# Optimization experiments

Measured on AMD Instinct MI355X. Metric: run time of the kernel, lower is better.

Reference implementation:

```python
import jax, jax.numpy as jnp
import numpy as np

D_MODEL = 1024
NUM_HEADS = 16
D_K = D_MODEL // NUM_HEADS
THETA = 10000.0
B, S = 2, 2048


def setup_inputs() -> dict:
    key = jax.random.key(0)
    k_x, k_q, k_k, k_v, k_o = jax.random.split(key, 5)
    std = np.sqrt(2.0 / (D_MODEL + D_MODEL))
    x = jax.random.normal(k_x, (B, S, D_MODEL), dtype=jnp.float32)
    # positions: per-row arange 0..S-1 (must stay < max_seq_len)
    token_positions = jnp.broadcast_to(jnp.arange(S, dtype=jnp.int32), (B, S))
    mk = lambda k: (jax.random.normal(k, (D_MODEL, D_MODEL), dtype=jnp.float32) * std)
    return {
        'x': x,
        'token_positions': token_positions,
        'Wq': mk(k_q), 'Wk': mk(k_k), 'Wv': mk(k_v), 'Wo': mk(k_o),
    }


def _rope(x, pos):
    # x: [B, H, S, D_K], pos: [B, S] int
    inv_freq = 1.0 / (THETA ** (jnp.arange(0, D_K, 2, dtype=jnp.float32) / D_K))  # [D_K/2]
    angles = pos.astype(jnp.float32)[..., None] * inv_freq  # [B, S, D_K/2]
    cos = jnp.cos(angles)[:, None, :, :]  # [B, 1, S, D_K/2]
    sin = jnp.sin(angles)[:, None, :, :]
    x_even = x[..., 0::2]
    x_odd = x[..., 1::2]
    out_even = x_even * cos - x_odd * sin
    out_odd = x_even * sin + x_odd * cos
    # interleave back: [..., D_K/2, 2] -> [..., D_K]
    return jnp.stack([out_even, out_odd], axis=-1).reshape(x.shape)


def reference(x, token_positions, Wq, Wk, Wv, Wo):
    b, s, d = x.shape
    h, dk = NUM_HEADS, D_K
    # projections: weight is [d_out, d_in], y = x W^T
    q = jnp.einsum('bsd,ed->bse', x, Wq).reshape(b, s, h, dk).transpose(0, 2, 1, 3)
    k = jnp.einsum('bsd,ed->bse', x, Wk).reshape(b, s, h, dk).transpose(0, 2, 1, 3)
    v = jnp.einsum('bsd,ed->bse', x, Wv).reshape(b, s, h, dk).transpose(0, 2, 1, 3)
    q = _rope(q, token_positions)
    k = _rope(k, token_positions)
    scores = jnp.einsum('bhqd,bhkd->bhqk', q, k) / jnp.sqrt(jnp.float32(dk))
    causal = jnp.tril(jnp.ones((s, s), dtype=bool))
    scores = jnp.where(causal, scores, -jnp.inf)
    weights = jax.nn.softmax(scores, axis=-1)
    attn = jnp.einsum('bhqk,bhkd->bhqd', weights, v)  # [B,H,S,D_K]
    concat = attn.transpose(0, 2, 1, 3).reshape(b, s, d)
    return jnp.einsum('bsd,ed->bse', concat, Wo)
```

## Files before the change

### kernel.cpp

```cpp
#include <hip/hip_runtime.h>
#include <hip/hip_bf16.h>

#define BB 2
#define SS 2048
#define DD 1024
#define HH 16
#define DKK 64
#define MM (BB * SS)
#define PER ((size_t)MM * DD)

typedef __bf16 v8bf __attribute__((ext_vector_type(8)));
typedef float  v4f  __attribute__((ext_vector_type(4)));

__device__ __forceinline__ float bf2f(unsigned int u16) {
    union { unsigned int i; float f; } x;
    x.i = u16 << 16;
    return x.f;
}
__device__ __forceinline__ unsigned int pack2(float a, float b) {
    union { __hip_bfloat16 h; unsigned short u; } x, y;
    x.h = __float2bfloat16(a); y.h = __float2bfloat16(b);
    return (unsigned int)x.u | ((unsigned int)y.u << 16);
}
__device__ __forceinline__ unsigned short f2bfu(float v) {
    union { __hip_bfloat16 h; unsigned short u; } x;
    x.h = __float2bfloat16(v);
    return x.u;
}
template<bool BF>
__device__ __forceinline__ void ld4(const void* p, size_t i, float* f) {
    if (BF) {
        const uint2 u = *(const uint2*)((const unsigned short*)p + i);
        f[0] = bf2f(u.x & 0xffffu); f[1] = bf2f(u.x >> 16);
        f[2] = bf2f(u.y & 0xffffu); f[3] = bf2f(u.y >> 16);
    } else {
        const float4 v = *(const float4*)((const float*)p + i);
        f[0] = v.x; f[1] = v.y; f[2] = v.z; f[3] = v.w;
    }
}
template<bool BF>
__device__ __forceinline__ void st1(void* p, size_t i, float v) {
    if (BF) ((__hip_bfloat16*)p)[i] = __float2bfloat16(v);
    else    ((float*)p)[i] = v;
}
template<bool BF>
__device__ __forceinline__ uint4 ld8bf(const void* p, size_t i) {
    if (BF) return *(const uint4*)((const unsigned short*)p + i);
    float f[8];
    ld4<false>(p, i, f);
    ld4<false>(p, i + 4, f + 4);
    uint4 u;
    u.x = pack2(f[0], f[1]); u.y = pack2(f[2], f[3]);
    u.z = pack2(f[4], f[5]); u.w = pack2(f[6], f[7]);
    return u;
}

typedef const __attribute__((address_space(1))) void* gas_p;
typedef __attribute__((address_space(3))) void* las_p;
__device__ __forceinline__ void gld16(const void* g, void* l) {
    __builtin_amdgcn_global_load_lds(
        (gas_p)(unsigned long long)g,
        (las_p)(unsigned int)(unsigned long long)l,
        16, 0, 0);
}

__device__ __forceinline__ bool sniff_bf(const void* x) {
    const unsigned int w = ((const unsigned int*)x)[threadIdx.x & 63];
    const int e = (w >> 7) & 0xFF;
    return __popcll(__ballot(e >= 100 && e <= 140)) >= 32;
}

__global__ __launch_bounds__(256) void precast(
    const void* __restrict__ X,  const void* __restrict__ Wq,
    const void* __restrict__ Wk, const void* __restrict__ Wv,
    const void* __restrict__ Wo, unsigned short* __restrict__ out)
{
    const int bid = blockIdx.x;
    const int tid = threadIdx.x;
    const void* src;
    size_t off;
    unsigned short* dst;
    if (bid < 2048) {
        src = X;
        off = (size_t)bid * 2048;
        dst = out + off;
    } else {
        const int w  = (bid - 2048) >> 9;
        const size_t lo = (size_t)((bid - 2048) & 511) * 2048;
        src = (w == 0) ? Wq : (w == 1) ? Wk : (w == 2) ? Wv : Wo;
        off = lo;
        dst = out + PER + (size_t)w * (DD * DD) + lo;
    }
    const bool bf = sniff_bf(src);
    const size_t i = off + (size_t)tid * 8;
    if (bf) {
        *(uint4*)(dst + tid * 8) = *(const uint4*)((const unsigned short*)src + i);
    } else {
        float f[8];
        ld4<false>(src, i, f);
        ld4<false>(src, i + 4, f + 4);
        uint4 u;
        u.x = pack2(f[0], f[1]); u.y = pack2(f[2], f[3]);
        u.z = pack2(f[4], f[5]); u.w = pack2(f[6], f[7]);
        *(uint4*)(dst + tid * 8) = u;
    }
}

template<bool BF>
__device__ __forceinline__ void qkv_body128(
    const void* __restrict__ X,
    const void* __restrict__ Wq, const void* __restrict__ Wk, const void* __restrict__ Wv,
    const int* __restrict__ pos,
    __hip_bfloat16* __restrict__ Qb, __hip_bfloat16* __restrict__ Kb,
    __hip_bfloat16* __restrict__ Vb,
    unsigned short* Sh)
{
    const int tid  = threadIdx.x;
    const int lane = tid & 63;
    const int wv   = tid >> 6;
    const int wr   = wv >> 1;
    const int wc   = wv & 1;
    const int ln   = lane & 15;
    const int qd   = lane >> 4;
    const int r8   = lane >> 3;
    const int pc   = lane & 7;
    const int lchunk = pc ^ r8;

    const int m0  = blockIdx.x * 128;
    const int n0g = blockIdx.y * 128;
    const int z   = n0g >> 10;
    const int nw  = n0g & (DD - 1);
    const void* W = (z == 0) ? Wq : (z == 1) ? Wk : Wv;

    unsigned short* As = Sh;
    unsigned short* Bs = Sh + 128 * 64;

    v4f acc[4][4];
#pragma unroll
    for (int i = 0; i < 4; ++i)
#pragma unroll
        for (int j = 0; j < 4; ++j) acc[i][j] = (v4f){0.f, 0.f, 0.f, 0.f};

    for (int k0 = 0; k0 < DD; k0 += 64) {
        __syncthreads();
#pragma unroll
        for (int g = 0; g < 4; ++g) {
            const int base = (wv * 4 + g) * 8;
            const int row  = base + r8;
            const size_t ga = (size_t)(m0 + row) * DD + k0 + lchunk * 8;
            if (BF) gld16((const unsigned short*)X + ga, As + (size_t)base * 64);
            else    *(uint4*)(As + (size_t)row * 64 + pc * 8) = ld8bf<false>(X, ga);
            const size_t gb = (size_t)(nw + row) * DD + k0 + lchunk * 8;
            if (BF) gld16((const unsigned short*)W + gb, Bs + (size_t)base * 64);
            else    *(uint4*)(Bs + (size_t)row * 64 + pc * 8) = ld8bf<false>(W, gb);
        }
        __syncthreads();
#pragma unroll
        for (int h = 0; h < 2; ++h) {
            v8bf a[4], b[4];
#pragma unroll
            for (int mt = 0; mt < 4; ++mt)
                a[mt] = *(const v8bf*)&As[(size_t)(wr * 64 + mt * 16 + ln) * 64 +
                                          (((h * 4 + qd) ^ (ln & 7))) * 8];
#pragma unroll
            for (int nt = 0; nt < 4; ++nt)
                b[nt] = *(const v8bf*)&Bs[(size_t)(wc * 64 + nt * 16 + ln) * 64 +
                                          (((h * 4 + qd) ^ (ln & 7))) * 8];
#pragma unroll
            for (int mt = 0; mt < 4; ++mt)
#pragma unroll
                for (int nt = 0; nt < 4; ++nt)
                    acc[mt][nt] = __builtin_amdgcn_mfma_f32_16x16x32_bf16(
                        a[mt], b[nt], acc[mt][nt], 0, 0, 0);
        }
    }

    const int bb = m0 >> 11;
    if (z < 2) {
        __hip_bfloat16* Out = z ? Kb : Qb;
        const int head = (nw >> 6) + wc;
        float invf[4];
#pragma unroll
        for (int nt = 0; nt < 4; ++nt) {
            const int dk = nt * 16 + ln;
            invf[nt] = __expf((float)(dk >> 1) * -0.2878231366f);
        }
#pragma unroll
        for (int mt = 0; mt < 4; ++mt) {
#pragma unroll
            for (int r = 0; r < 4; ++r) {
                const int m = m0 + wr * 64 + mt * 16 + qd * 4 + r;
                const int s = m & (SS - 1);
                const float p = (float)pos[m];
#pragma unroll
                for (int nt = 0; nt < 4; ++nt) {
                    const int dk = nt * 16 + ln;
                    const float val = acc[mt][nt][r];
                    const float ang = p * invf[nt];
                    float sn, cs;
                    __sincosf(ang, &sn, &cs);
                    const float prt = __shfl_xor(val, 1);
                    float res = ((dk & 1) == 0) ? (val * cs - prt * sn)
                                                : (prt * sn + val * cs);
                    if (z == 0) res *= 0.125f;
                    Out[((size_t)(bb * HH + head) * SS + s) * DKK + dk] =
                        __float2bfloat16(res);
                }
            }
        }
    } else {
        const int s0 = m0 & (SS - 1);
#pragma unroll
        for (int h2 = 0; h2 < 2; ++h2) {
            __syncthreads();
            if (wc == h2) {
#pragma unroll
                for (int nt = 0; nt < 4; ++nt)
#pragma unroll
                    for (int mt = 0; mt < 4; ++mt)
#pragma unroll
                        for (int r = 0; r < 4; ++r)
                            Sh[(size_t)(nt * 16 + ln) * 136 +
                               wr * 64 + mt * 16 + qd * 4 + r] =
                                f2bfu(acc[mt][nt][r]);
            }
            __syncthreads();
            const int head = (nw >> 6) + h2;
            const int row  = tid >> 2;
            const int c    = (tid & 3) * 32;
            unsigned short* dst = (unsigned short*)Vb +
                ((size_t)(bb * HH + head) * DKK + row) * SS + s0 + c;
            const unsigned short* Ts = Sh + (size_t)row * 136 + c;
#pragma unroll
            for (int j = 0; j < 4; ++j)
                *(uint4*)(dst + j * 8) = *(const uint4*)(Ts + j * 8);
        }
    }
}

__global__ __launch_bounds__(256) void qkv_gemm(
    const void* __restrict__ X,
    const void* __restrict__ Wq, const void* __restrict__ Wk, const void* __restrict__ Wv,
    const int* __restrict__ pos,
    __hip_bfloat16* __restrict__ Qb, __hip_bfloat16* __restrict__ Kb,
    __hip_bfloat16* __restrict__ Vb)
{
    __shared__ unsigned short Sh[128 * 64 * 2];
    if (sniff_bf(X)) qkv_body128<true>(X, Wq, Wk, Wv, pos, Qb, Kb, Vb, Sh);
    else             qkv_body128<false>(X, Wq, Wk, Wv, pos, Qb, Kb, Vb, Sh);
}

__global__ __launch_bounds__(256) void qkv_gemm_pc(
    const unsigned short* __restrict__ Xb,
    const unsigned short* __restrict__ Wqb, const unsigned short* __restrict__ Wkb,
    const unsigned short* __restrict__ Wvb,
    const int* __restrict__ pos,
    __hip_bfloat16* __restrict__ Qb, __hip_bfloat16* __restrict__ Kb,
    __hip_bfloat16* __restrict__ Vb)
{
    __shared__ unsigned short Sh[128 * 64 * 2];
    qkv_body128<true>(Xb, Wqb, Wkb, Wvb, pos, Qb, Kb, Vb, Sh);
}

__global__ __launch_bounds__(256) void attn_kernel(
    const __hip_bfloat16* __restrict__ Qb,
    const __hip_bfloat16* __restrict__ Kb,
    const __hip_bfloat16* __restrict__ Vtb,
    unsigned short* __restrict__ Ob, int olay)
{
    __shared__ unsigned short Ks[2][64 * 64];
    __shared__ unsigned short Vs[2][64 * 64];
    __shared__ unsigned short Ps[4][16 * 72];

    const int tid  = threadIdx.x;
    const int bh   = blockIdx.x & 31;
    const int qt   = 31 - (blockIdx.x >> 5);
    const int q0   = qt * 64;
    const int lane = tid & 63;
    const int wv   = tid >> 6;
    const int ln   = lane & 15;
    const int qd   = lane >> 4;
    const int r8   = lane >> 3;
    const int pc   = lane & 7;
    const int lchunk = pc ^ r8;

    const unsigned short* Qu = (const unsigned short*)Qb + (size_t)bh * SS * DKK;
    const unsigned short* Ku = (const unsigned short*)Kb + (size_t)bh * SS * DKK;
    const unsigned short* Vu = (const unsigned short*)Vtb + (size_t)bh * DKK * SS;

    const int qrow = q0 + wv * 16 + ln;
    const v8bf qf0 = *(const v8bf*)(Qu + (size_t)qrow * DKK + qd * 8);
    const v8bf qf1 = *(const v8bf*)(Qu + (size_t)qrow * DKK + 32 + qd * 8);

    auto stage = [&](int t, int b) {
        const int k0 = t * 64;
#pragma unroll
        for (int g = 0; g < 2; ++g) {
            const int row  = wv * 16 + g * 8 + r8;
            const int base = wv * 16 + g * 8;
            gld16(Ku + (size_t)(k0 + row) * DKK + lchunk * 8,
                  Ks[b] + (size_t)base * 64);
            gld16(Vu + (size_t)row * SS + k0 + lchunk * 8,
                  Vs[b] + (size_t)base * 64);
        }
    };

    v4f oacc[4];
#pragma unroll
    for (int n = 0; n < 4; ++n) oacc[n] = (v4f){0.f, 0.f, 0.f, 0.f};
    float lsum = 0.f;

    const int ntiles = qt + 1;
    const int qi = q0 + wv * 16 + ln;

    stage(0, 0);
    __syncthreads();

    for (int t = 0; t < ntiles; ++t) {
        const int cur = t & 1;
        if (t + 1 < ntiles) stage(t + 1, cur ^ 1);

        const unsigned short* Kc = Ks[cur];
        const unsigned short* Vc = Vs[cur];

        v4f s[4];
        __builtin_amdgcn_s_setprio(1);
#pragma unroll
        for (int g = 0; g < 4; ++g) {
            s[g] = (v4f){0.f, 0.f, 0.f, 0.f};
            const int krow = g * 16 + ln;
            const v8bf kf0 = *(const v8bf*)&Kc[(size_t)krow * 64 + ((qd ^ (ln & 7))) * 8];
            const v8bf kf1 = *(const v8bf*)&Kc[(size_t)krow * 64 + (((4 + qd) ^ (ln & 7))) * 8];
            s[g] = __builtin_amdgcn_mfma_f32_16x16x32_bf16(kf0, qf0, s[g], 0, 0, 0);
            s[g] = __builtin_amdgcn_mfma_f32_16x16x32_bf16(kf1, qf1, s[g], 0, 0, 0);
        }
        __builtin_amdgcn_s_setprio(0);

        const int k0 = t * 64;
        if (t == qt) {
#pragma unroll
            for (int g = 0; g < 4; ++g)
#pragma unroll
                for (int r = 0; r < 4; ++r) {
                    const int key = k0 + g * 16 + qd * 4 + r;
                    const float sv = (key <= qi) ? s[g][r] : -1e30f;
                    const float p = __expf(sv - 20.f);
                    s[g][r] = p;
                    lsum += p;
                }
        } else {
#pragma unroll
            for (int g = 0; g < 4; ++g)
#pragma unroll
                for (int r = 0; r < 4; ++r) {
                    const float p = __expf(s[g][r] - 20.f);
                    s[g][r] = p;
                    lsum += p;
                }
        }

        unsigned short* Pw = Ps[wv];
#pragma unroll
        for (int g = 0; g < 4; ++g) {
            uint2 w;
            w.x = pack2(s[g][0], s[g][1]);
            w.y = pack2(s[g][2], s[g][3]);
            *(uint2*)&Pw[(size_t)ln * 72 + g * 16 + qd * 4] = w;
        }

        const v8bf pf0 = *(const v8bf*)&Pw[(size_t)ln * 72 + qd * 8];
        const v8bf pf1 = *(const v8bf*)&Pw[(size_t)ln * 72 + 32 + qd * 8];
        __builtin_amdgcn_s_setprio(1);
#pragma unroll
        for (int n = 0; n < 4; ++n) {
            const int vrow = n * 16 + ln;
            const v8bf vf0 = *(const v8bf*)&Vc[(size_t)vrow * 64 + ((qd ^ (ln & 7))) * 8];
            const v8bf vf1 = *(const v8bf*)&Vc[(size_t)vrow * 64 + (((4 + qd) ^ (ln & 7))) * 8];
            oacc[n] = __builtin_amdgcn_mfma_f32_16x16x32_bf16(pf0, vf0, oacc[n], 0, 0, 0);
            oacc[n] = __builtin_amdgcn_mfma_f32_16x16x32_bf16(pf1, vf1, oacc[n], 0, 0, 0);
        }
        __builtin_amdgcn_s_setprio(0);

        __syncthreads();
    }

    lsum += __shfl_xor(lsum, 16);
    lsum += __shfl_xor(lsum, 32);

#pragma unroll
    for (int r = 0; r < 4; ++r) {
        const float inv = 1.f / __shfl(lsum, qd * 4 + r);
        const int row = q0 + wv * 16 + qd * 4 + r;
        unsigned short* op;
        if (olay) {
            op = Ob + ((size_t)((bh >> 4) * SS + row)) * DD + (bh & 15) * DKK;
        } else {
            op = Ob + ((size_t)bh * SS + row) * DKK;
        }
#pragma unroll
        for (int n = 0; n < 4; ++n)
            op[n * 16 + ln] = f2bfu(oacc[n][r] * inv);
    }
}

template<bool BFB, bool BFO, bool ACONT>
__device__ __forceinline__ void out_body128(
    const __hip_bfloat16* __restrict__ Ab, const void* __restrict__ Wo,
    void* __restrict__ Cb, float* __restrict__ Cf, int raw,
    unsigned short* Sh)
{
    const int tid  = threadIdx.x;
    const int lane = tid & 63;
    const int wv   = tid >> 6;
    const int wr   = wv >> 1;
    const int wc   = wv & 1;
    const int ln   = lane & 15;
    const int qd   = lane >> 4;
    const int r8   = lane >> 3;
    const int pc   = lane & 7;
    const int lchunk = pc ^ r8;

    const int m0 = blockIdx.x * 128, n0 = blockIdx.y * 128;
    const unsigned short* Au = (const unsigned short*)Ab;

    unsigned short* Abuf[2] = { Sh,               Sh + 2 * 8192 };
    unsigned short* Bbuf[2] = { Sh + 8192,        Sh + 3 * 8192 };

    auto stage = [&](int k0, unsigned short* Ad, unsigned short* Bd) {
#pragma unroll
        for (int g = 0; g < 4; ++g) {
            const int base = (wv * 4 + g) * 8;
            const int row  = base + r8;
            const int m = m0 + row;
            size_t ga;
            if (ACONT) ga = (size_t)m * DD + k0 + lchunk * 8;
            else       ga = ((size_t)((m >> 11) * HH + (k0 >> 6)) * SS + (m & (SS - 1))) * DKK
                            + lchunk * 8;
            gld16(Au + ga, Ad + (size_t)base * 64);
            const size_t gb = (size_t)(n0 + row) * DD + k0 + lchunk * 8;
            if (BFB) gld16((const unsigned short*)Wo + gb, Bd + (size_t)base * 64);
            else     *(uint4*)(Bd + (size_t)row * 64 + pc * 8) = ld8bf<false>(Wo, gb);
        }
    };

    v4f acc[4][4];
#pragma unroll
    for (int i = 0; i < 4; ++i)
#pragma unroll
        for (int j = 0; j < 4; ++j) acc[i][j] = (v4f){0.f, 0.f, 0.f, 0.f};

    stage(0, Abuf[0], Bbuf[0]);
    __syncthreads();

    for (int kk = 0; kk < 16; ++kk) {
        const int cur = kk & 1;
        if (kk + 1 < 16) stage((kk + 1) * 64, Abuf[cur ^ 1], Bbuf[cur ^ 1]);

        const unsigned short* As = Abuf[cur];
        const unsigned short* Bs = Bbuf[cur];
#pragma unroll
        for (int h = 0; h < 2; ++h) {
            v8bf a[4], b[4];
#pragma unroll
            for (int mt = 0; mt < 4; ++mt)
                a[mt] = *(const v8bf*)&As[(size_t)(wr * 64 + mt * 16 + ln) * 64 +
                                          (((h * 4 + qd) ^ (ln & 7))) * 8];
#pragma unroll
            for (int nt = 0; nt < 4; ++nt)
                b[nt] = *(const v8bf*)&Bs[(size_t)(wc * 64 + nt * 16 + ln) * 64 +
                                          (((h * 4 + qd) ^ (ln & 7))) * 8];
#pragma unroll
            for (int mt = 0; mt < 4; ++mt)
#pragma unroll
                for (int nt = 0; nt < 4; ++nt)
                    acc[mt][nt] = __builtin_amdgcn_mfma_f32_16x16x32_bf16(
                        a[mt], b[nt], acc[mt][nt], 0, 0, 0);
        }
        __syncthreads();
    }

#pragma unroll
    for (int mt = 0; mt < 4; ++mt) {
#pragma unroll
        for (int r = 0; r < 4; ++r) {
            const int m = m0 + wr * 64 + mt * 16 + qd * 4 + r;
#pragma unroll
            for (int nt = 0; nt < 4; ++nt) {
                const int e = n0 + wc * 64 + nt * 16 + ln;
                const size_t idx = (size_t)m * DD + e;
                const float v = acc[mt][nt][r];
                if (raw) Cf[idx] = v;
                else     st1<BFO>(Cb, idx, v);
            }
        }
    }
}

__global__ __launch_bounds__(256) void out_gemm(
    const __hip_bfloat16* __restrict__ Ab, const void* __restrict__ Wo,
    void* __restrict__ Cb, float* __restrict__ Cf, int raw,
    const void* __restrict__ xs)
{
    __shared__ unsigned short Sh[4 * 8192];
    if (sniff_bf(xs)) out_body128<true,  true,  false>(Ab, Wo, Cb, Cf, raw, Sh);
    else              out_body128<false, false, false>(Ab, Wo, Cb, Cf, raw, Sh);
}

__global__ __launch_bounds__(256) void out_gemm_pc(
    const __hip_bfloat16* __restrict__ Ab, const unsigned short* __restrict__ Wob,
    void* __restrict__ Cb, const void* __restrict__ xs)
{
    __shared__ unsigned short Sh[4 * 8192];
    if (sniff_bf(xs)) out_body128<true, true,  true>(Ab, Wob, Cb, nullptr, 0, Sh);
    else              out_body128<true, false, true>(Ab, Wob, Cb, nullptr, 0, Sh);
}

__global__ __launch_bounds__(256) void copy_cast(
    const float* __restrict__ src, void* __restrict__ dst, const void* __restrict__ xs)
{
    const bool bf = sniff_bf(xs);
    const size_t i = (size_t)blockIdx.x * 256 + threadIdx.x;
    const float v = src[i];
    if (bf) ((__hip_bfloat16*)dst)[i] = __float2bfloat16(v);
    else    ((float*)dst)[i] = v;
}

extern "C" void kernel_launch(void* const* d_in, const int* in_sizes, int n_in,
                              void* d_out, int out_size, void* d_ws, size_t ws_size,
                              hipStream_t stream) {
    (void)in_sizes; (void)n_in; (void)out_size;

    const void* x   = d_in[0];
    const int*  pos = (const int*)d_in[1];
    const void* Wq  = d_in[2];
    const void* Wk  = d_in[3];
    const void* Wv  = d_in[4];
    const void* Wo  = d_in[5];

    char* ws = (char*)d_ws;
    const size_t bpb   = PER * 2;
    const size_t wcast = (size_t)DD * DD * 2;
    const size_t need_full = 3 * bpb + bpb + 4 * wcast + 64;

    if (ws_size >= need_full) {
        __hip_bfloat16* Qb = (__hip_bfloat16*)ws;
        __hip_bfloat16* Kb = Qb + PER;
        __hip_bfloat16* Vb = Kb + PER;
        unsigned short* cast = (unsigned short*)(ws + 3 * bpb);
        unsigned short* Xb  = cast;
        unsigned short* Wqb = cast + PER;
        unsigned short* Wkb = Wqb + (size_t)DD * DD;
        unsigned short* Wvb = Wkb + (size_t)DD * DD;
        unsigned short* Wob = Wvb + (size_t)DD * DD;
        unsigned short* Obuf = Xb;

        precast<<<dim3(4096), 256, 0, stream>>>(x, Wq, Wk, Wv, Wo, cast);

        dim3 g1(MM / 128, (3 * DD) / 128);
        qkv_gemm_pc<<<g1, 256, 0, stream>>>(Xb, Wqb, Wkb, Wvb, pos, Qb, Kb, Vb);

        dim3 g2(32 * 32);
        attn_kernel<<<g2, 256, 0, stream>>>(Qb, Kb, Vb, Obuf, 1);

        dim3 g3(MM / 128, DD / 128);
        out_gemm_pc<<<g3, 256, 0, stream>>>((const __hip_bfloat16*)Obuf, Wob, d_out, x);
    } else if (ws_size >= 3 * bpb + 64) {
        __hip_bfloat16* Qb = (__hip_bfloat16*)ws;
        __hip_bfloat16* Kb = Qb + PER;
        __hip_bfloat16* Vb = Kb + PER;

        dim3 g1(MM / 128, (3 * DD) / 128);
        qkv_gemm<<<g1, 256, 0, stream>>>(x, Wq, Wk, Wv, pos, Qb, Kb, Vb);

        dim3 g2(32 * 32);
        attn_kernel<<<g2, 256, 0, stream>>>(Qb, Kb, Vb, (unsigned short*)Qb, 0);

        dim3 g3(MM / 128, DD / 128);
        out_gemm<<<g3, 256, 0, stream>>>(Qb, Wo, d_out, nullptr, 0, x);
    } else {
        __hip_bfloat16* Qb = (__hip_bfloat16*)d_out;
        __hip_bfloat16* Kb = (__hip_bfloat16*)ws;
        __hip_bfloat16* Vb = Kb + PER;
        float* Cf = (float*)ws;

        dim3 g1(MM / 128, (3 * DD) / 128);
        qkv_gemm<<<g1, 256, 0, stream>>>(x, Wq, Wk, Wv, pos, Qb, Kb, Vb);

        dim3 g2(32 * 32);
        attn_kernel<<<g2, 256, 0, stream>>>(Qb, Kb, Vb, (unsigned short*)Qb, 0);

        dim3 g3(MM / 128, DD / 128);
        out_gemm<<<g3, 256, 0, stream>>>(Qb, Wo, nullptr, Cf, 1, x);

        copy_cast<<<PER / 256, 256, 0, stream>>>(Cf, d_out, x);
    }
}
```

Baseline: 178.2 us.

## Double-buffer QKV GEMM K-loop and use precomputed RoPE sin/cos table

Restructures the QKV projection GEMM main loop to use 32-wide K tiles with double-buffered LDS, prefetching the next tile while MFMAs run on the current one, with one barrier per iteration instead of two. It also adds extra blocks to the precast kernel that fill a position-by-frequency cos/sin table, which the GEMM epilogue reads in place of computing exp and sincos per element. This is meant to hide global-to-LDS load latency and to cut transcendental work in the epilogue. In exchange the K loop runs twice as many iterations on smaller tiles, and the epilogue now does scattered table loads.

```diff
diff --git a/kernel.cpp b/kernel.cpp
--- a/kernel.cpp
+++ b/kernel.cpp
@@ -73,10 +73,24 @@
 __global__ __launch_bounds__(256) void precast(
     const void* __restrict__ X,  const void* __restrict__ Wq,
     const void* __restrict__ Wk, const void* __restrict__ Wv,
-    const void* __restrict__ Wo, unsigned short* __restrict__ out)
+    const void* __restrict__ Wo, unsigned short* __restrict__ out,
+    float* __restrict__ tab)
 {
     const int bid = blockIdx.x;
     const int tid = threadIdx.x;
+
+    if (bid >= 4096) {
+        const int idx = (bid - 4096) * 256 + tid;
+        const int s = idx >> 5;
+        const int f = idx & 31;
+        const float invf = __expf((float)f * -0.2878231366f);
+        const float ang = (float)s * invf;
+        float sn, cs;
+        __sincosf(ang, &sn, &cs);
+        ((float2*)tab)[idx] = make_float2(cs, sn);
+        return;
+    }
+
     const void* src;
     size_t off;
     unsigned short* dst;
@@ -106,11 +120,11 @@
     }
 }
 
-template<bool BF>
+template<bool BF, bool TAB>
 __device__ __forceinline__ void qkv_body128(
     const void* __restrict__ X,
     const void* __restrict__ Wq, const void* __restrict__ Wk, const void* __restrict__ Wv,
-    const int* __restrict__ pos,
+    const int* __restrict__ pos, const float* __restrict__ tab,
     __hip_bfloat16* __restrict__ Qb, __hip_bfloat16* __restrict__ Kb,
     __hip_bfloat16* __restrict__ Vb,
     unsigned short* Sh)
@@ -122,9 +136,8 @@
     const int wc   = wv & 1;
     const int ln   = lane & 15;
     const int qd   = lane >> 4;
-    const int r8   = lane >> 3;
-    const int pc   = lane & 7;
-    const int lchunk = pc ^ r8;
+    const int srow = lane >> 2;
+    const int sc4  = lane & 3;
 
     const int m0  = blockIdx.x * 128;
     const int n0g = blockIdx.y * 128;
@@ -132,8 +145,25 @@
     const int nw  = n0g & (DD - 1);
     const void* W = (z == 0) ? Wq : (z == 1) ? Wk : Wv;
 
-    unsigned short* As = Sh;
-    unsigned short* Bs = Sh + 128 * 64;
+    unsigned short* A0 = Sh;
+    unsigned short* A1 = Sh + 4096;
+    unsigned short* B0 = Sh + 8192;
+    unsigned short* B1 = Sh + 12288;
+
+    auto stage = [&](int k0, unsigned short* Ad, unsigned short* Bd) {
+#pragma unroll
+        for (int g = 0; g < 2; ++g) {
+            const int base = (wv * 2 + g) * 16;
+            const int row  = base + srow;
+            const int sc   = sc4 ^ ((row >> 1) & 3);
+            const size_t ga = (size_t)(m0 + row) * DD + k0 + sc * 8;
+            if (BF) gld16((const unsigned short*)X + ga, Ad + (size_t)base * 32);
+            else    *(uint4*)(Ad + (size_t)row * 32 + sc4 * 8) = ld8bf<false>(X, ga);
+            const size_t gb = (size_t)(nw + row) * DD + k0 + sc * 8;
+            if (BF) gld16((const unsigned short*)W + gb, Bd + (size_t)base * 32);
+            else    *(uint4*)(Bd + (size_t)row * 32 + sc4 * 8) = ld8bf<false>(W, gb);
+        }
+    };
 
     v4f acc[4][4];
 #pragma unroll
@@ -141,38 +171,35 @@
 #pragma unroll
         for (int j = 0; j < 4; ++j) acc[i][j] = (v4f){0.f, 0.f, 0.f, 0.f};
 
-    for (int k0 = 0; k0 < DD; k0 += 64) {
+    unsigned short *Ac = A0, *An = A1, *Bc = B0, *Bn = B1;
+    stage(0, Ac, Bc);
+    __syncthreads();
+
+    const int rsw = (ln >> 1) & 3;
+
+    for (int t = 0; t < 32; ++t) {
+        if (t + 1 < 32) stage((t + 1) * 32, An, Bn);
+
+        v8bf a[4], b[4];
+#pragma unroll
+        for (int mt = 0; mt < 4; ++mt)
+            a[mt] = *(const v8bf*)&Ac[(size_t)(wr * 64 + mt * 16 + ln) * 32 +
+                                      ((qd ^ rsw)) * 8];
+#pragma unroll
+        for (int nt = 0; nt < 4; ++nt)
+            b[nt] = *(const v8bf*)&Bc[(size_t)(wc * 64 + nt * 16 + ln) * 32 +
+                                      ((qd ^ rsw)) * 8];
+#pragma unroll
+        for (int mt = 0; mt < 4; ++mt)
+#pragma unroll
+            for (int nt = 0; nt < 4; ++nt)
+                acc[mt][nt] = __builtin_amdgcn_mfma_f32_16x16x32_bf16(
+                    a[mt], b[nt], acc[mt][nt], 0, 0, 0);
+
         __syncthreads();
-#pragma unroll
-        for (int g = 0; g < 4; ++g) {
-            const int base = (wv * 4 + g) * 8;
-            const int row  = base + r8;
-            const size_t ga = (size_t)(m0 + row) * DD + k0 + lchunk * 8;
-            if (BF) gld16((const unsigned short*)X + ga, As + (size_t)base * 64);
-            else    *(uint4*)(As + (size_t)row * 64 + pc * 8) = ld8bf<false>(X, ga);
-            const size_t gb = (size_t)(nw + row) * DD + k0 + lchunk * 8;
-            if (BF) gld16((const unsigned short*)W + gb, Bs + (size_t)base * 64);
-            else    *(uint4*)(Bs + (size_t)row * 64 + pc * 8) = ld8bf<false>(W, gb);
-        }
-        __syncthreads();
-#pragma unroll
-        for (int h = 0; h < 2; ++h) {
-            v8bf a[4], b[4];
-#pragma unroll
-            for (int mt = 0; mt < 4; ++mt)
-                a[mt] = *(const v8bf*)&As[(size_t)(wr * 64 + mt * 16 + ln) * 64 +
-                                          (((h * 4 + qd) ^ (ln & 7))) * 8];
-#pragma unroll
-            for (int nt = 0; nt < 4; ++nt)
-                b[nt] = *(const v8bf*)&Bs[(size_t)(wc * 64 + nt * 16 + ln) * 64 +
-                                          (((h * 4 + qd) ^ (ln & 7))) * 8];
-#pragma unroll
-            for (int mt = 0; mt < 4; ++mt)
-#pragma unroll
-                for (int nt = 0; nt < 4; ++nt)
-                    acc[mt][nt] = __builtin_amdgcn_mfma_f32_16x16x32_bf16(
-                        a[mt], b[nt], acc[mt][nt], 0, 0, 0);
-        }
+        unsigned short* tp;
+        tp = Ac; Ac = An; An = tp;
+        tp = Bc; Bc = Bn; Bn = tp;
     }
 
     const int bb = m0 >> 11;
@@ -180,10 +207,12 @@
         __hip_bfloat16* Out = z ? Kb : Qb;
         const int head = (nw >> 6) + wc;
         float invf[4];
-#pragma unroll
-        for (int nt = 0; nt < 4; ++nt) {
-            const int dk = nt * 16 + ln;
-            invf[nt] = __expf((float)(dk >> 1) * -0.2878231366f);
+        if (!TAB) {
+#pragma unroll
+            for (int nt = 0; nt < 4; ++nt) {
+                const int dk = nt * 16 + ln;
+                invf[nt] = __expf((float)(dk >> 1) * -0.2878231366f);
+            }
         }
 #pragma unroll
         for (int mt = 0; mt < 4; ++mt) {
@@ -191,14 +220,22 @@
             for (int r = 0; r < 4; ++r) {
                 const int m = m0 + wr * 64 + mt * 16 + qd * 4 + r;
                 const int s = m & (SS - 1);
-                const float p = (float)pos[m];
+                const int pi = pos[m];
+                const float p = (float)pi;
+                const float2* trow = TAB ? ((const float2*)tab) + (size_t)pi * 32
+                                         : nullptr;
 #pragma unroll
                 for (int nt = 0; nt < 4; ++nt) {
                     const int dk = nt * 16 + ln;
                     const float val = acc[mt][nt][r];
-                    const float ang = p * invf[nt];
                     float sn, cs;
-                    __sincosf(ang, &sn, &cs);
+                    if (TAB) {
+                        const float2 t2 = trow[nt * 8 + (ln >> 1)];
+                        cs = t2.x; sn = t2.y;
+                    } else {
+                        const float ang = p * invf[nt];
+                        __sincosf(ang, &sn, &cs);
+                    }
                     const float prt = __shfl_xor(val, 1);
                     float res = ((dk & 1) == 0) ? (val * cs - prt * sn)
                                                 : (prt * sn + val * cs);
@@ -245,21 +282,21 @@
     __hip_bfloat16* __restrict__ Qb, __hip_bfloat16* __restrict__ Kb,
     __hip_bfloat16* __restrict__ Vb)
 {
-    __shared__ unsigned short Sh[128 * 64 * 2];
-    if (sniff_bf(X)) qkv_body128<true>(X, Wq, Wk, Wv, pos, Qb, Kb, Vb, Sh);
-    else             qkv_body128<false>(X, Wq, Wk, Wv, pos, Qb, Kb, Vb, Sh);
+    __shared__ unsigned short Sh[16384];
+    if (sniff_bf(X)) qkv_body128<true,  false>(X, Wq, Wk, Wv, pos, nullptr, Qb, Kb, Vb, Sh);
+    else             qkv_body128<false, false>(X, Wq, Wk, Wv, pos, nullptr, Qb, Kb, Vb, Sh);
 }
 
 __global__ __launch_bounds__(256) void qkv_gemm_pc(
     const unsigned short* __restrict__ Xb,
     const unsigned short* __restrict__ Wqb, const unsigned short* __restrict__ Wkb,
     const unsigned short* __restrict__ Wvb,
-    const int* __restrict__ pos,
+    const int* __restrict__ pos, const float* __restrict__ tab,
     __hip_bfloat16* __restrict__ Qb, __hip_bfloat16* __restrict__ Kb,
     __hip_bfloat16* __restrict__ Vb)
 {
-    __shared__ unsigned short Sh[128 * 64 * 2];
-    qkv_body128<true>(Xb, Wqb, Wkb, Wvb, pos, Qb, Kb, Vb, Sh);
+    __shared__ unsigned short Sh[16384];
+    qkv_body128<true, true>(Xb, Wqb, Wkb, Wvb, pos, tab, Qb, Kb, Vb, Sh);
 }
 
 __global__ __launch_bounds__(256) void attn_kernel(
@@ -539,8 +576,9 @@
 
     char* ws = (char*)d_ws;
     const size_t bpb   = PER * 2;
-    const size_t wcast = (size_t)DD * DD * 2;
-    const size_t need_full = 3 * bpb + bpb + 4 * wcast + 64;
+    const size_t castb = (PER + 4 * (size_t)DD * DD) * 2;
+    const size_t tabb  = (size_t)SS * 32 * 2 * sizeof(float);
+    const size_t need_full = 3 * bpb + castb + tabb + 64;
 
     if (ws_size >= need_full) {
         __hip_bfloat16* Qb = (__hip_bfloat16*)ws;
@@ -552,12 +590,13 @@
         unsigned short* Wkb = Wqb + (size_t)DD * DD;
         unsigned short* Wvb = Wkb + (size_t)DD * DD;
         unsigned short* Wob = Wvb + (size_t)DD * DD;
+        float* tab = (float*)(cast + PER + 4 * (size_t)DD * DD);
         unsigned short* Obuf = Xb;
 
-        precast<<<dim3(4096), 256, 0, stream>>>(x, Wq, Wk, Wv, Wo, cast);
+        precast<<<dim3(4352), 256, 0, stream>>>(x, Wq, Wk, Wv, Wo, cast, tab);
 
         dim3 g1(MM / 128, (3 * DD) / 128);
-        qkv_gemm_pc<<<g1, 256, 0, stream>>>(Xb, Wqb, Wkb, Wvb, pos, Qb, Kb, Vb);
+        qkv_gemm_pc<<<g1, 256, 0, stream>>>(Xb, Wqb, Wkb, Wvb, pos, tab, Qb, Kb, Vb);
 
         dim3 g2(32 * 32);
         attn_kernel<<<g2, 256, 0, stream>>>(Qb, Kb, Vb, Obuf, 1);
```

After: 182.9 us. 2.6% more time.
